# Performance work log

Measured on AMD Instinct MI355X. Metric: run time of the kernel, lower is better.

Reference implementation:

```python
import jax, jax.numpy as jnp
import numpy as np

B, N, CIN, COUT, K, E = 8, 50000, 64, 64, 3, 400000


def setup_inputs() -> dict:
    key = jax.random.key(0)
    k0, k1, k2, k3 = jax.random.split(key, 4)
    x = jax.random.normal(k0, (B, N, CIN), dtype=jnp.float32)
    weight = jax.random.normal(k1, (K, CIN, COUT), dtype=jnp.float32) * 0.05
    bias = jax.random.normal(k2, (COUT,), dtype=jnp.float32) * 0.05
    edge_index = jax.random.randint(k3, (2, E), 0, N, dtype=jnp.int64)
    return {"x": x, "weight": weight, "bias": bias, "edge_index": edge_index}


def reference(x, weight, bias, edge_index):
    b, n, cin = x.shape
    k_order = weight.shape[0]
    row, col = edge_index[0], edge_index[1]
    # remove self loops (edge_weight defaults to ones)
    ew = jnp.where(row != col, jnp.float32(1.0), jnp.float32(0.0))
    deg = jax.ops.segment_sum(ew, row, num_segments=n)
    dinv = jnp.where(deg > 0, deg ** -0.5, 0.0)
    lap = -dinv[row] * ew * dinv[col]  # [E]

    def prop(t):  # sparse lap @ t along node dim; t: [B, N, Cin]
        tn = t.transpose(1, 0, 2).reshape(n, -1)            # [N, B*Cin]
        y = jax.ops.segment_sum(lap[:, None] * tn[col], row, num_segments=n)
        return y.reshape(n, b, cin).transpose(1, 0, 2)       # [B, N, Cin]

    tx0 = x
    out = jnp.einsum('bni,io->bno', tx0, weight[0])
    if k_order > 1:
        tx1 = prop(x)
        out = out + jnp.einsum('bni,io->bno', tx1, weight[1])
    for k in range(2, k_order):
        tx2 = 2.0 * prop(tx1) - tx0
        out = out + jnp.einsum('bni,io->bno', tx2, weight[k])
        tx0, tx1 = tx1, tx2
    return out + bias
```

## Files before the change

kernel.cpp:

```cpp
#include <hip/hip_runtime.h>

#define NB 8
#define NN 50000
#define NC 64
#define NE 400000

typedef unsigned short us4 __attribute__((ext_vector_type(4)));
typedef unsigned short us8 __attribute__((ext_vector_type(8)));
typedef short s8v __attribute__((ext_vector_type(8)));
typedef float f4v __attribute__((ext_vector_type(4)));

__device__ __forceinline__ float bf2f(unsigned short u) {
  union { unsigned int i; float f; } v; v.i = ((unsigned int)u) << 16; return v.f;
}
__device__ __forceinline__ unsigned short f2bf(float f) {
  union { float f; unsigned int i; } v; v.f = f;
  unsigned int x = v.i;
  return (unsigned short)((x + 0x7FFFu + ((x >> 16) & 1u)) >> 16);
}
__device__ __forceinline__ void fma4(float4& a, float s, const float4& v) {
  a.x = fmaf(s, v.x, a.x); a.y = fmaf(s, v.y, a.y);
  a.z = fmaf(s, v.z, a.z); a.w = fmaf(s, v.w, a.w);
}

__device__ __forceinline__ void gather_group(
    const unsigned short* __restrict__ tb, const int2* __restrict__ edges,
    int s, int e, int lane, int2 myed, float (&acc)[8]) {
  int jc = s;
  while (jc < e) {
    int take = e - jc; if (take > 64) take = 64;
    if (jc != s) myed = edges[jc + (lane < take ? lane : take - 1)];
    int full = take & ~7;
    int m = 0;
    for (; m < full; m += 8) {
      us8 v[8]; float lp[8];
#pragma unroll
      for (int u = 0; u < 8; ++u) {
        int c = __shfl(myed.x, m + u, 64);
        lp[u] = __int_as_float(__shfl(myed.y, m + u, 64));
        v[u] = *(const us8*)&tb[(size_t)c * 512];
      }
#pragma unroll
      for (int u = 0; u < 8; ++u)
#pragma unroll
        for (int q = 0; q < 8; ++q) acc[q] = fmaf(lp[u], bf2f(v[u][q]), acc[q]);
    }
    if (m < take) {
      int rem = take - m;
      us8 v[8]; float lp[8];
#pragma unroll
      for (int u = 0; u < 8; ++u) {
        if (u < rem) {
          int c = __shfl(myed.x, m + u, 64);
          lp[u] = __int_as_float(__shfl(myed.y, m + u, 64));
          v[u] = *(const us8*)&tb[(size_t)c * 512];
        }
      }
#pragma unroll
      for (int u = 0; u < 8; ++u) {
        if (u < rem) {
#pragma unroll
          for (int q = 0; q < 8; ++q) acc[q] = fmaf(lp[u], bf2f(v[u][q]), acc[q]);
        }
      }
    }
    jc += take;
  }
}

__global__ void cheb_count(const int* __restrict__ ei, int* __restrict__ cnt) {
  int e = blockIdx.x * blockDim.x + threadIdx.x;
  if (e >= NE) return;
  int r = ei[e], c = ei[NE + e];
  if (r != c) atomicAdd(&cnt[r], 1);
}

__global__ void cheb_offsets(const int* __restrict__ cnt, float* __restrict__ dinv,
                             int* __restrict__ rowptr, int* __restrict__ cur,
                             int* __restrict__ total) {
  int n = blockIdx.x * blockDim.x + threadIdx.x;
  if (n >= NN) return;
  int c = cnt[n];
  dinv[n] = (c > 0) ? rsqrtf((float)c) : 0.0f;
  int s = atomicAdd(total, c);
  rowptr[n] = s;
  cur[n] = s;
}

__global__ void cheb_scatter(const int* __restrict__ ei, const float* __restrict__ dinv,
                             int* __restrict__ cur, int2* __restrict__ edges) {
  int e = blockIdx.x * blockDim.x + threadIdx.x;
  if (e >= NE) return;
  int r = ei[e], c = ei[NE + e];
  if (r == c) return;
  int pos = atomicAdd(&cur[r], 1);
  float lap = -dinv[r] * dinv[c];
  edges[pos] = make_int2(c, __float_as_int(lap));
}

__global__ void cheb_wc(const float* __restrict__ w, float* __restrict__ wc) {
  int i = blockIdx.x * blockDim.x + threadIdx.x;
  if (i >= NC * NC) return;
  float w0 = w[i];
  float w1 = w[NC * NC + i];
  float w2 = w[2 * NC * NC + i];
  wc[i] = w0 - w2;
  wc[NC * NC + i] = w1;
  wc[2 * NC * NC + i] = 2.0f * w2;
}

__global__ void cheb_wpack(const float* __restrict__ w, unsigned short* __restrict__ pack) {
  int t = blockIdx.x * blockDim.x + threadIdx.x;
  if (t >= 6 * 4 * 64 * 8) return;
  int jj = t & 7;
  int l  = (t >> 3) & 63;
  int nt = (t >> 9) & 3;
  int ks = t >> 11;
  int k = ks * 32 + ((l >> 4) * 8) + jj;
  int o = nt * 16 + (l & 15);
  int ki = k & 63, ch = k >> 6;
  float v;
  if (ch == 0)      v = w[ki * 64 + o] - w[2 * 4096 + ki * 64 + o];
  else if (ch == 1) v = w[4096 + ki * 64 + o];
  else              v = 2.0f * w[2 * 4096 + ki * 64 + o];
  pack[t] = f2bf(v);
}

__global__ __launch_bounds__(256) void cheb_convert(
    const float* __restrict__ x, unsigned short* __restrict__ xh) {
  int t = blockIdx.x * blockDim.x + threadIdx.x;
  if (t >= NN * 128) return;
  int n = t >> 7;
  int rem = t & 127;
  int b = rem >> 4;
  int c4 = (rem & 15) * 4;
  f4v v = __builtin_nontemporal_load((const f4v*)&x[((size_t)b * NN + n) * 64 + c4]);
  us4 o;
  o[0] = f2bf(v[0]); o[1] = f2bf(v[1]); o[2] = f2bf(v[2]); o[3] = f2bf(v[3]);
  *(us4*)&xh[(size_t)n * 512 + b * 64 + c4] = o;
}

__global__ __launch_bounds__(256) void cheb_prop1h(
    const unsigned short* __restrict__ tin, unsigned short* __restrict__ tout,
    const int* __restrict__ rowptr, const int* __restrict__ cnt,
    const int2* __restrict__ edges) {
  int n = (blockIdx.x << 2) + (threadIdx.x >> 6);
  if (n >= NN) return;
  int lane = threadIdx.x & 63;
  int s = rowptr[n], c = cnt[n];
  const unsigned short* tb = tin + lane * 8;
  float acc[8];
#pragma unroll
  for (int q = 0; q < 8; ++q) acc[q] = 0.0f;
  if (c > 0) {
    int t0 = c > 64 ? 64 : c;
    int2 myed = edges[s + (lane < t0 ? lane : t0 - 1)];
    gather_group(tb, edges, s, s + c, lane, myed, acc);
  }
  us8 o;
#pragma unroll
  for (int q = 0; q < 8; ++q) o[q] = f2bf(acc[q]);
  *(us8*)&tout[(size_t)n * 512 + lane * 8] = o;
}

__global__ __launch_bounds__(256) void cheb_fused(
    const unsigned short* __restrict__ xh, const unsigned short* __restrict__ tx1h,
    const int* __restrict__ rowptr, const int* __restrict__ cnt,
    const int2* __restrict__ edges, const unsigned short* __restrict__ pack,
    const float* __restrict__ bias, float* __restrict__ out) {
  __shared__ unsigned short Pb[4][32][72];
  int w = threadIdx.x >> 6, lane = threadIdx.x & 63;
  int row0 = blockIdx.x * 128 + w * 32;
  int n0 = row0 >> 3;
  unsigned short (*P)[72] = Pb[w];

  int sj[4], cj[4];
#pragma unroll
  for (int j = 0; j < 4; ++j) { sj[j] = rowptr[n0 + j]; cj[j] = cnt[n0 + j]; }
  int2 med[4];
#pragma unroll
  for (int j = 0; j < 4; ++j) {
    int t0 = cj[j] > 64 ? 64 : cj[j];
    int idx = (t0 > 0) ? (sj[j] + (lane < t0 ? lane : t0 - 1)) : 0;
    med[j] = edges[idx];
  }

  const unsigned short* tb = tx1h + lane * 8;
  for (int j = 0; j < 4; ++j) {
    float acc8[8];
#pragma unroll
    for (int q = 0; q < 8; ++q) acc8[q] = 0.0f;
    if (cj[j] > 0)
      gather_group(tb, edges, sj[j], sj[j] + cj[j], lane, med[j], acc8);
    us8 o;
#pragma unroll
    for (int q = 0; q < 8; ++q) o[q] = f2bf(acc8[q]);
    *(us8*)&P[j * 8 + (lane >> 3)][(lane & 7) * 8] = o;
  }

  f4v acc[2][4];
#pragma unroll
  for (int mt = 0; mt < 2; ++mt)
#pragma unroll
    for (int nt = 0; nt < 4; ++nt) acc[mt][nt] = (f4v){0.f, 0.f, 0.f, 0.f};

  int am = lane & 15, aq = (lane >> 4) * 8;
#pragma unroll
  for (int ks = 0; ks < 6; ++ks) {
    s8v a0, a1;
    if (ks < 2) {
      a0 = __builtin_nontemporal_load((const s8v*)&xh[(size_t)(row0 + am) * 64 + ks * 32 + aq]);
      a1 = __builtin_nontemporal_load((const s8v*)&xh[(size_t)(row0 + 16 + am) * 64 + ks * 32 + aq]);
    } else if (ks < 4) {
      a0 = __builtin_nontemporal_load((const s8v*)&tx1h[(size_t)(row0 + am) * 64 + (ks - 2) * 32 + aq]);
      a1 = __builtin_nontemporal_load((const s8v*)&tx1h[(size_t)(row0 + 16 + am) * 64 + (ks - 2) * 32 + aq]);
    } else {
      a0 = *(const s8v*)&P[am][(ks - 4) * 32 + aq];
      a1 = *(const s8v*)&P[16 + am][(ks - 4) * 32 + aq];
    }
#pragma unroll
    for (int nt = 0; nt < 4; ++nt) {
      s8v b = *(const s8v*)&pack[(((size_t)(ks * 4 + nt) * 64) + lane) * 8];
      acc[0][nt] = __builtin_amdgcn_mfma_f32_16x16x32_bf16(a0, b, acc[0][nt], 0, 0, 0);
      acc[1][nt] = __builtin_amdgcn_mfma_f32_16x16x32_bf16(a1, b, acc[1][nt], 0, 0, 0);
    }
  }

  float bv[4];
#pragma unroll
  for (int nt = 0; nt < 4; ++nt) bv[nt] = bias[nt * 16 + (lane & 15)];
#pragma unroll
  for (int mt = 0; mt < 2; ++mt)
#pragma unroll
    for (int r = 0; r < 4; ++r) {
      int rl = mt * 16 + (lane >> 4) * 4 + r;
      int rn = row0 + rl;
      int b = rn & 7, nn = rn >> 3;
      float* orow = &out[((size_t)b * NN + nn) * 64 + (lane & 15)];
#pragma unroll
      for (int nt = 0; nt < 4; ++nt)
        __builtin_nontemporal_store(acc[mt][nt][r] + bv[nt], &orow[nt * 16]);
    }
}

__global__ __launch_bounds__(256) void cheb_prop(
    const float* __restrict__ tin, float* __restrict__ tout,
    const int* __restrict__ rowptr, const int* __restrict__ cnt,
    const int2* __restrict__ edges, int nwaves) {
  int wid = (blockIdx.x << 2) + (threadIdx.x >> 6);
  if (wid >= nwaves) return;
  int lane = threadIdx.x & 63;
  int b = wid / NN;
  int n = wid - b * NN;
  int s = rowptr[n];
  int e = s + cnt[n];
  const float* base = tin + (size_t)b * NN * NC;
  float acc = 0.0f;
  for (int j = s; j < e; ++j) {
    int2 ed = edges[j];
    acc += __int_as_float(ed.y) * base[(size_t)ed.x * NC + lane];
  }
  tout[((size_t)b * NN + n) * NC + lane] = acc;
}

__global__ __launch_bounds__(256) void cheb_gemm2(
    const float* __restrict__ x, const float* __restrict__ tx1,
    const float* ptx1, const float* __restrict__ wc,
    const float* __restrict__ bias, float* out, int nrows) {
  __shared__ float At[128][64];
  __shared__ float Ws[64][64];
  int tid = threadIdx.x;
  int tx = tid & 15;
  int ty = tid >> 4;
  long row0 = (long)blockIdx.x * 128;
  int sk4 = (tid & 15) * 4;
  int srb = tid >> 4;
  const float* sp[3] = {x, tx1, ptx1};
  float4 pa[8], pw[4];
  auto fetch = [&](int ch) {
    const float* s0 = sp[ch];
#pragma unroll
    for (int rr = 0; rr < 8; ++rr) {
      int roff = srb + rr * 16;
      if (row0 + roff < nrows)
        pa[rr] = *(const float4*)&s0[(size_t)(row0 + roff) * NC + sk4];
      else
        pa[rr] = make_float4(0.f, 0.f, 0.f, 0.f);
    }
#pragma unroll
    for (int ww = 0; ww < 4; ++ww) {
      int e4 = tid + 256 * ww;
      pw[ww] = *(const float4*)&wc[ch * 4096 + (e4 >> 4) * 64 + (e4 & 15) * 4];
    }
  };
  auto commit = [&]() {
#pragma unroll
    for (int rr = 0; rr < 8; ++rr)
      *(float4*)&At[srb + rr * 16][sk4] = pa[rr];
#pragma unroll
    for (int ww = 0; ww < 4; ++ww) {
      int e4 = tid + 256 * ww;
      *(float4*)&Ws[e4 >> 4][(e4 & 15) * 4] = pw[ww];
    }
  };
  float4 acc[8];
#pragma unroll
  for (int i = 0; i < 8; ++i) acc[i] = make_float4(0.f, 0.f, 0.f, 0.f);
  fetch(0);
  commit();
  for (int ch = 0; ch < 3; ++ch) {
    __syncthreads();
    if (ch < 2) fetch(ch + 1);
#pragma unroll 4
    for (int k4 = 0; k4 < 16; ++k4) {
      float4 w0 = *(float4*)&Ws[k4 * 4 + 0][tx * 4];
      float4 w1 = *(float4*)&Ws[k4 * 4 + 1][tx * 4];
      float4 w2 = *(float4*)&Ws[k4 * 4 + 2][tx * 4];
      float4 w3 = *(float4*)&Ws[k4 * 4 + 3][tx * 4];
#pragma unroll
      for (int i = 0; i < 8; ++i) {
        float4 a = *(float4*)&At[ty * 8 + i][k4 * 4];
        fma4(acc[i], a.x, w0);
        fma4(acc[i], a.y, w1);
        fma4(acc[i], a.z, w2);
        fma4(acc[i], a.w, w3);
      }
    }
    __syncthreads();
    if (ch < 2) commit();
  }
  float4 bb4 = *(const float4*)&bias[tx * 4];
#pragma unroll
  for (int i = 0; i < 8; ++i) {
    long r = row0 + ty * 8 + i;
    if (r >= nrows) continue;
    float4 o = make_float4(acc[i].x + bb4.x, acc[i].y + bb4.y,
                           acc[i].z + bb4.z, acc[i].w + bb4.w);
    *(float4*)&out[(size_t)r * NC + tx * 4] = o;
  }
}

extern "C" void kernel_launch(void* const* d_in, const int* in_sizes, int n_in,
                              void* d_out, int out_size, void* d_ws, size_t ws_size,
                              hipStream_t stream) {
  (void)in_sizes; (void)n_in; (void)out_size;
  const float* x    = (const float*)d_in[0];
  const float* w    = (const float*)d_in[1];
  const float* bias = (const float*)d_in[2];
  const int*   ei   = (const int*)d_in[3];
  float* out = (float*)d_out;
  char* ws = (char*)d_ws;

  size_t off = 0;
  auto alloc = [&](size_t bytes) -> void* {
    void* p = (void*)(ws + off);
    off = (off + bytes + 255) & ~(size_t)255;
    return p;
  };
  int* cnt      = (int*)alloc((size_t)(NN + 1) * sizeof(int));
  int* total    = cnt + NN;
  int* rowptr   = (int*)alloc((size_t)NN * sizeof(int));
  int* cur      = (int*)alloc((size_t)NN * sizeof(int));
  float* dinv   = (float*)alloc((size_t)NN * sizeof(float));
  int2* edges   = (int2*)alloc((size_t)NE * sizeof(int2));
  float* wcb    = (float*)alloc((size_t)3 * NC * NC * sizeof(float));
  unsigned short* pack = (unsigned short*)alloc((size_t)6 * 4 * 64 * 8 * sizeof(unsigned short));
  size_t small_end = off;

  hipMemsetAsync(cnt, 0, (NN + 1) * sizeof(int), stream);
  cheb_count  <<<(NE + 255) / 256, 256, 0, stream>>>(ei, cnt);
  cheb_offsets<<<(NN + 255) / 256, 256, 0, stream>>>(cnt, dinv, rowptr, cur, total);
  cheb_scatter<<<(NE + 255) / 256, 256, 0, stream>>>(ei, dinv, cur, edges);

  const size_t fieldHB = (size_t)NN * 512 * sizeof(unsigned short);
  const size_t perbB   = (size_t)NN * NC * sizeof(float);

  if (ws_size >= small_end + 2 * fieldHB + 256) {
    unsigned short* xh   = (unsigned short*)alloc(fieldHB);
    unsigned short* tx1h = (unsigned short*)alloc(fieldHB);
    cheb_wpack  <<<(6 * 4 * 64 * 8 + 255) / 256, 256, 0, stream>>>(w, pack);
    cheb_convert<<<(NN * 128) / 256, 256, 0, stream>>>(x, xh);
    cheb_prop1h <<<NN / 4, 256, 0, stream>>>(xh, tx1h, rowptr, cnt, edges);
    cheb_fused  <<<(NB * NN) / 128, 256, 0, stream>>>(
        xh, tx1h, rowptr, cnt, edges, pack, bias, out);
  } else if (ws_size >= small_end + 2 * perbB + 256) {
    cheb_wc<<<(NC * NC + 255) / 256, 256, 0, stream>>>(w, wcb);
    float* tx1b  = (float*)alloc(perbB);
    float* ptx1b = (float*)alloc(perbB);
    for (int b = 0; b < NB; ++b) {
      const float* xb = x + (size_t)b * NN * NC;
      float* outb = out + (size_t)b * NN * NC;
      cheb_prop<<<(NN + 3) / 4, 256, 0, stream>>>(xb, tx1b, rowptr, cnt, edges, NN);
      cheb_prop<<<(NN + 3) / 4, 256, 0, stream>>>(tx1b, ptx1b, rowptr, cnt, edges, NN);
      cheb_gemm2<<<(NN + 127) / 128, 256, 0, stream>>>(
          xb, tx1b, ptx1b, wcb, bias, outb, NN);
    }
  } else {
    cheb_wc<<<(NC * NC + 255) / 256, 256, 0, stream>>>(w, wcb);
    float* tx1b = (float*)alloc(perbB);
    for (int b = 0; b < NB; ++b) {
      const float* xb = x + (size_t)b * NN * NC;
      float* outb = out + (size_t)b * NN * NC;
      cheb_prop<<<(NN + 3) / 4, 256, 0, stream>>>(xb, tx1b, rowptr, cnt, edges, NN);
      cheb_prop<<<(NN + 3) / 4, 256, 0, stream>>>(tx1b, outb, rowptr, cnt, edges, NN);
      cheb_gemm2<<<(NN + 127) / 128, 256, 0, stream>>>(
          xb, tx1b, outb, wcb, bias, outb, NN);
    }
  }
}
```

Before: 372.8 us.

## Software-pipeline neighbor gathers across four nodes per wave and wave-scan offsets

Adds a double-buffered gather routine that issues the first batch of neighbor row loads for the next node while accumulating the current node. Both the first-hop propagation kernel, now four nodes per wave, and the fused kernel use it. This is meant to hide gather latency that the serialized per-node loop exposed. The offsets kernel also replaces per-node atomics with a wave prefix scan plus one atomic per wave. The costs are higher register pressure from the two buffers and fewer waves in the propagation kernel.

```diff
diff --git a/kernel.cpp b/kernel.cpp
--- a/kernel.cpp
+++ b/kernel.cpp
@@ -21,6 +21,45 @@
 __device__ __forceinline__ void fma4(float4& a, float s, const float4& v) {
   a.x = fmaf(s, v.x, a.x); a.y = fmaf(s, v.y, a.y);
   a.z = fmaf(s, v.z, a.z); a.w = fmaf(s, v.w, a.w);
+}
+
+__device__ __forceinline__ void issue8(const unsigned short* __restrict__ tb,
+                                       int2 myed, int m, int take, us8 (&v)[8]) {
+  int rem = take - m; if (rem > 8) rem = 8;
+  if (rem == 8) {
+#pragma unroll
+    for (int u = 0; u < 8; ++u) {
+      int c = __shfl(myed.x, m + u, 64);
+      v[u] = *(const us8*)&tb[(size_t)c * 512];
+    }
+  } else {
+#pragma unroll
+    for (int u = 0; u < 8; ++u)
+      if (u < rem) {
+        int c = __shfl(myed.x, m + u, 64);
+        v[u] = *(const us8*)&tb[(size_t)c * 512];
+      }
+  }
+}
+__device__ __forceinline__ void consume8(int2 myed, int m, int take,
+                                         const us8 (&v)[8], float (&acc)[8]) {
+  int rem = take - m; if (rem > 8) rem = 8;
+  if (rem == 8) {
+#pragma unroll
+    for (int u = 0; u < 8; ++u) {
+      float l = __int_as_float(__shfl(myed.y, m + u, 64));
+#pragma unroll
+      for (int q = 0; q < 8; ++q) acc[q] = fmaf(l, bf2f(v[u][q]), acc[q]);
+    }
+  } else {
+#pragma unroll
+    for (int u = 0; u < 8; ++u)
+      if (u < rem) {
+        float l = __int_as_float(__shfl(myed.y, m + u, 64));
+#pragma unroll
+        for (int q = 0; q < 8; ++q) acc[q] = fmaf(l, bf2f(v[u][q]), acc[q]);
+      }
+  }
 }
 
 __device__ __forceinline__ void gather_group(
@@ -30,41 +69,56 @@
   while (jc < e) {
     int take = e - jc; if (take > 64) take = 64;
     if (jc != s) myed = edges[jc + (lane < take ? lane : take - 1)];
-    int full = take & ~7;
-    int m = 0;
-    for (; m < full; m += 8) {
-      us8 v[8]; float lp[8];
-#pragma unroll
-      for (int u = 0; u < 8; ++u) {
-        int c = __shfl(myed.x, m + u, 64);
-        lp[u] = __int_as_float(__shfl(myed.y, m + u, 64));
-        v[u] = *(const us8*)&tb[(size_t)c * 512];
+    for (int m = 0; m < take; m += 8) {
+      us8 v[8];
+      issue8(tb, myed, m, take, v);
+      consume8(myed, m, take, v, acc);
+    }
+    jc += take;
+  }
+}
+
+template <typename EmitFn>
+__device__ __forceinline__ void prop4_pipelined(
+    const unsigned short* __restrict__ tb, const int2* __restrict__ edges,
+    const int* __restrict__ rowptr, const int* __restrict__ cnt,
+    int n0, int lane, EmitFn emit) {
+  int sj[4], cj[4], tj[4];
+#pragma unroll
+  for (int j = 0; j < 4; ++j) {
+    sj[j] = rowptr[n0 + j]; cj[j] = cnt[n0 + j];
+    tj[j] = cj[j] > 64 ? 64 : cj[j];
+  }
+  int2 med[4];
+#pragma unroll
+  for (int j = 0; j < 4; ++j) {
+    int idx = (tj[j] > 0) ? (sj[j] + (lane < tj[j] ? lane : tj[j] - 1)) : 0;
+    med[j] = edges[idx];
+  }
+  us8 va[8], vb[8];
+  if (tj[0] > 0) issue8(tb, med[0], 0, tj[0], va);
+#pragma unroll
+  for (int j = 0; j < 4; ++j) {
+    us8 (&curv)[8] = (j & 1) ? vb : va;
+    us8 (&nxtv)[8] = (j & 1) ? va : vb;
+    if (j < 3 && tj[j + 1] > 0) issue8(tb, med[j + 1], 0, tj[j + 1], nxtv);
+    float acc8[8];
+#pragma unroll
+    for (int q = 0; q < 8; ++q) acc8[q] = 0.0f;
+    if (tj[j] > 0) {
+      consume8(med[j], 0, tj[j], curv, acc8);
+      for (int m = 8; m < tj[j]; m += 8) {
+        issue8(tb, med[j], m, tj[j], curv);
+        consume8(med[j], m, tj[j], curv, acc8);
       }
-#pragma unroll
-      for (int u = 0; u < 8; ++u)
-#pragma unroll
-        for (int q = 0; q < 8; ++q) acc[q] = fmaf(lp[u], bf2f(v[u][q]), acc[q]);
-    }
-    if (m < take) {
-      int rem = take - m;
-      us8 v[8]; float lp[8];
-#pragma unroll
-      for (int u = 0; u < 8; ++u) {
-        if (u < rem) {
-          int c = __shfl(myed.x, m + u, 64);
-          lp[u] = __int_as_float(__shfl(myed.y, m + u, 64));
-          v[u] = *(const us8*)&tb[(size_t)c * 512];
-        }
+      if (cj[j] > 64) {
+        int rs = sj[j] + 64, re = sj[j] + cj[j];
+        int t = re - rs; if (t > 64) t = 64;
+        int2 m2 = edges[rs + (lane < t ? lane : t - 1)];
+        gather_group(tb, edges, rs, re, lane, m2, acc8);
       }
-#pragma unroll
-      for (int u = 0; u < 8; ++u) {
-        if (u < rem) {
-#pragma unroll
-          for (int q = 0; q < 8; ++q) acc[q] = fmaf(lp[u], bf2f(v[u][q]), acc[q]);
-        }
-      }
-    }
-    jc += take;
+    }
+    emit(j, acc8);
   }
 }
 
@@ -79,12 +133,25 @@
                              int* __restrict__ rowptr, int* __restrict__ cur,
                              int* __restrict__ total) {
   int n = blockIdx.x * blockDim.x + threadIdx.x;
-  if (n >= NN) return;
-  int c = cnt[n];
-  dinv[n] = (c > 0) ? rsqrtf((float)c) : 0.0f;
-  int s = atomicAdd(total, c);
-  rowptr[n] = s;
-  cur[n] = s;
+  int lane = threadIdx.x & 63;
+  bool valid = n < NN;
+  int c = valid ? cnt[n] : 0;
+  int inc = c;
+#pragma unroll
+  for (int d = 1; d < 64; d <<= 1) {
+    int t = __shfl_up(inc, d, 64);
+    if (lane >= d) inc += t;
+  }
+  int wtot = __shfl(inc, 63, 64);
+  int base = 0;
+  if (lane == 63) base = atomicAdd(total, wtot);
+  base = __shfl(base, 63, 64);
+  int s = base + inc - c;
+  if (valid) {
+    dinv[n] = (c > 0) ? rsqrtf((float)c) : 0.0f;
+    rowptr[n] = s;
+    cur[n] = s;
+  }
 }
 
 __global__ void cheb_scatter(const int* __restrict__ ei, const float* __restrict__ dinv,
@@ -144,23 +211,18 @@
     const unsigned short* __restrict__ tin, unsigned short* __restrict__ tout,
     const int* __restrict__ rowptr, const int* __restrict__ cnt,
     const int2* __restrict__ edges) {
-  int n = (blockIdx.x << 2) + (threadIdx.x >> 6);
-  if (n >= NN) return;
+  int wv = (blockIdx.x << 2) + (threadIdx.x >> 6);
+  int n0 = wv * 4;
+  if (n0 >= NN) return;
   int lane = threadIdx.x & 63;
-  int s = rowptr[n], c = cnt[n];
   const unsigned short* tb = tin + lane * 8;
-  float acc[8];
-#pragma unroll
-  for (int q = 0; q < 8; ++q) acc[q] = 0.0f;
-  if (c > 0) {
-    int t0 = c > 64 ? 64 : c;
-    int2 myed = edges[s + (lane < t0 ? lane : t0 - 1)];
-    gather_group(tb, edges, s, s + c, lane, myed, acc);
-  }
-  us8 o;
-#pragma unroll
-  for (int q = 0; q < 8; ++q) o[q] = f2bf(acc[q]);
-  *(us8*)&tout[(size_t)n * 512 + lane * 8] = o;
+  prop4_pipelined(tb, edges, rowptr, cnt, n0, lane,
+                  [&](int j, float (&acc8)[8]) {
+    us8 o;
+#pragma unroll
+    for (int q = 0; q < 8; ++q) o[q] = f2bf(acc8[q]);
+    *(us8*)&tout[(size_t)(n0 + j) * 512 + lane * 8] = o;
+  });
 }
 
 __global__ __launch_bounds__(256) void cheb_fused(
@@ -174,29 +236,14 @@
   int n0 = row0 >> 3;
   unsigned short (*P)[72] = Pb[w];
 
-  int sj[4], cj[4];
-#pragma unroll
-  for (int j = 0; j < 4; ++j) { sj[j] = rowptr[n0 + j]; cj[j] = cnt[n0 + j]; }
-  int2 med[4];
-#pragma unroll
-  for (int j = 0; j < 4; ++j) {
-    int t0 = cj[j] > 64 ? 64 : cj[j];
-    int idx = (t0 > 0) ? (sj[j] + (lane < t0 ? lane : t0 - 1)) : 0;
-    med[j] = edges[idx];
-  }
-
   const unsigned short* tb = tx1h + lane * 8;
-  for (int j = 0; j < 4; ++j) {
-    float acc8[8];
-#pragma unroll
-    for (int q = 0; q < 8; ++q) acc8[q] = 0.0f;
-    if (cj[j] > 0)
-      gather_group(tb, edges, sj[j], sj[j] + cj[j], lane, med[j], acc8);
+  prop4_pipelined(tb, edges, rowptr, cnt, n0, lane,
+                  [&](int j, float (&acc8)[8]) {
     us8 o;
 #pragma unroll
     for (int q = 0; q < 8; ++q) o[q] = f2bf(acc8[q]);
     *(us8*)&P[j * 8 + (lane >> 3)][(lane & 7) * 8] = o;
-  }
+  });
 
   f4v acc[2][4];
 #pragma unroll
@@ -380,7 +427,7 @@
     unsigned short* tx1h = (unsigned short*)alloc(fieldHB);
     cheb_wpack  <<<(6 * 4 * 64 * 8 + 255) / 256, 256, 0, stream>>>(w, pack);
     cheb_convert<<<(NN * 128) / 256, 256, 0, stream>>>(x, xh);
-    cheb_prop1h <<<NN / 4, 256, 0, stream>>>(xh, tx1h, rowptr, cnt, edges);
+    cheb_prop1h <<<NN / 16, 256, 0, stream>>>(xh, tx1h, rowptr, cnt, edges);
     cheb_fused  <<<(NB * NN) / 128, 256, 0, stream>>>(
         xh, tx1h, rowptr, cnt, edges, pack, bias, out);
   } else if (ws_size >= small_end + 2 * perbB + 256) {
```

New measurement: 411.4 us. 1.1x slower.
